# Kernel optimization log

Hardware: AMD Instinct MI355X
Metric: run time of the kernel (lower is better)

## Reference

```python
import jax, jax.numpy as jnp
import numpy as np

B, T, C = 4, 1024, 1024
H, D = 16, 64


def setup_inputs() -> dict:
    key = jax.random.key(0)
    ks = jax.random.split(key, 5)
    sc = 0.02
    x = jax.random.normal(ks[0], (B, T, C), dtype=jnp.float32)
    Wq = jax.random.normal(ks[1], (H, C, D), dtype=jnp.float32) * sc
    Wk = jax.random.normal(ks[2], (H, C, D), dtype=jnp.float32) * sc
    Wv = jax.random.normal(ks[3], (H, C, D), dtype=jnp.float32) * sc
    Wp = jax.random.normal(ks[4], (H * D, C), dtype=jnp.float32) * sc
    bp = jnp.zeros((C,), dtype=jnp.float32)
    return {"x": x, "Wq": Wq, "Wk": Wk, "Wv": Wv, "Wp": Wp, "bp": bp}


def reference(x, Wq, Wk, Wv, Wp, bp):
    # per-head projections (bias-free, as in nanoGPT Head)
    q = jnp.einsum('btc,hcd->bhtd', x, Wq)
    k = jnp.einsum('btc,hcd->bhtd', x, Wk)
    v = jnp.einsum('btc,hcd->bhtd', x, Wv)
    scale = 1.0 / jnp.sqrt(jnp.asarray(D, dtype=x.dtype))
    scores = jnp.einsum('bhtd,bhsd->bhts', q, k) * scale  # [B,H,T,T]
    causal = jnp.tril(jnp.ones((T, T), dtype=bool))
    scores = jnp.where(causal, scores, jnp.asarray(-jnp.inf, dtype=scores.dtype))
    attn = jax.nn.softmax(scores, axis=-1)
    out = jnp.einsum('bhts,bhsd->bhtd', attn, v)  # [B,H,T,D]
    out = out.transpose(0, 2, 1, 3).reshape(B, T, H * D)  # concat heads
    return out @ Wp + bp  # final projection (dropout=0)
```

## Files before the change

### kernel.cpp

```cpp
#include <hip/hip_runtime.h>
#include <hip/hip_bf16.h>

typedef unsigned short u16;
typedef __bf16 bf16x8 __attribute__((ext_vector_type(8)));
typedef float floatx4 __attribute__((ext_vector_type(4)));

#define SB 4
#define ST 1024
#define SC 1024
#define SH 16
#define SD 64

__device__ __forceinline__ u16 f2bf(float f) {
    unsigned int u = __builtin_bit_cast(unsigned int, f);
    u += 0x7fffu + ((u >> 16) & 1u);
    return (u16)(u >> 16);
}

__device__ __forceinline__ void gload16(const u16* g, u16* l) {
    __builtin_amdgcn_global_load_lds(
        (const __attribute__((address_space(1))) unsigned int*)g,
        (__attribute__((address_space(3))) unsigned int*)l, 16, 0, 0);
}

__global__ void k_cvt_x(const float* __restrict__ x, u16* __restrict__ xb, int n4) {
    int i = blockIdx.x * blockDim.x + threadIdx.x;
    if (i < n4) {
        float4 v = ((const float4*)x)[i];
        uint2 o;
        o.x = (unsigned)f2bf(v.x) | ((unsigned)f2bf(v.y) << 16);
        o.y = (unsigned)f2bf(v.z) | ((unsigned)f2bf(v.w) << 16);
        ((uint2*)xb)[i] = o;
    }
}

__global__ void k_cvt_wqkv(const float* __restrict__ Wq, const float* __restrict__ Wk,
                           const float* __restrict__ Wv, u16* __restrict__ Wt) {
    __shared__ float tile[64][65];
    const int qkv = blockIdx.z, h = blockIdx.y, c0 = blockIdx.x * 64;
    const float* src = qkv == 0 ? Wq : (qkv == 1 ? Wk : Wv);
    #pragma unroll
    for (int i = 0; i < 16; ++i) {
        int idx = threadIdx.x + i * 256;
        int r = idx >> 6, d = idx & 63;
        tile[r][d] = src[(h * SC + c0 + r) * SD + d];
    }
    __syncthreads();
    #pragma unroll
    for (int i = 0; i < 16; ++i) {
        int idx = threadIdx.x + i * 256;
        int d = idx >> 6, cc = idx & 63;
        Wt[(qkv * 1024 + h * SD + d) * SC + c0 + cc] = f2bf(tile[cc][d]);
    }
}

__global__ void k_cvt_wp(const float* __restrict__ Wp, u16* __restrict__ Wt) {
    __shared__ float tile[64][65];
    const int n0 = blockIdx.x * 64, k0 = blockIdx.y * 64;
    #pragma unroll
    for (int i = 0; i < 16; ++i) {
        int idx = threadIdx.x + i * 256;
        int r = idx >> 6, nn = idx & 63;
        tile[r][nn] = Wp[(k0 + r) * SC + n0 + nn];
    }
    __syncthreads();
    #pragma unroll
    for (int i = 0; i < 16; ++i) {
        int idx = threadIdx.x + i * 256;
        int nr = idx >> 6, kk = idx & 63;
        Wt[(n0 + nr) * (SH * SD) + k0 + kk] = f2bf(tile[kk][nr]);
    }
}

__global__ void k_tv(const u16* __restrict__ V, u16* __restrict__ Vt) {
    __shared__ u16 tl[64 * 72];
    const int bh = blockIdx.y, t0 = blockIdx.x * 64;
    const int tid = threadIdx.x;
    #pragma unroll
    for (int i = 0; i < 2; ++i) {
        int idx = tid + i * 256;
        int r = idx >> 3, c = idx & 7;
        *(uint4*)&tl[r * 72 + c * 8] = *(const uint4*)&V[((long)bh * ST + t0 + r) * SD + c * 8];
    }
    __syncthreads();
    #pragma unroll
    for (int i = 0; i < 2; ++i) {
        int idx = tid + i * 256;
        int d = idx >> 3, tc = idx & 7;
        u16 tmp[8];
        #pragma unroll
        for (int e = 0; e < 8; ++e) tmp[e] = tl[(tc * 8 + e) * 72 + d];
        *(uint4*)&Vt[((long)bh * SD + d) * ST + t0 + tc * 8] = *(uint4*)tmp;
    }
}

template<int BN, int MODE>
__launch_bounds__(256)
__global__ void k_gemm(const u16* __restrict__ A, const u16* __restrict__ Bt,
                       int M, int N, int K,
                       u16* __restrict__ Qb, u16* __restrict__ Kb, u16* __restrict__ Vb,
                       const float* __restrict__ bias, float* __restrict__ Cout) {
    constexpr int SN = BN / 32, CB = BN / 32;
    __shared__ u16 Als[128 * 64];
    __shared__ u16 Bls[BN * 64];
    const int tid = threadIdx.x, lane = tid & 63, w = tid >> 6;
    const int quad = lane >> 4, l16 = lane & 15;
    const int sr = lane >> 3, sc = lane & 7;
    const int nt = N / BN;
    const int m0 = (blockIdx.x / nt) * 128, n0 = (blockIdx.x % nt) * BN;
    const int wm = (w >> 1) * 64, wn = (w & 1) * (BN / 2);

    floatx4 acc[4][SN] = {};
    for (int k0 = 0; k0 < K; k0 += 64) {
        #pragma unroll
        for (int i = 0; i < 4; ++i) {
            int rb = (w * 4 + i) * 8;
            gload16(&A[(long)(m0 + rb + sr) * K + k0 + ((sc ^ sr) << 3)], &Als[rb * 64]);
        }
        #pragma unroll
        for (int i = 0; i < CB; ++i) {
            int rb = (w * CB + i) * 8;
            gload16(&Bt[(long)(n0 + rb + sr) * K + k0 + ((sc ^ sr) << 3)], &Bls[rb * 64]);
        }
        __syncthreads();
        bf16x8 af[4][2], bfr[SN][2];
        #pragma unroll
        for (int sm = 0; sm < 4; ++sm) {
            int row = wm + sm * 16 + l16;
            #pragma unroll
            for (int ks = 0; ks < 2; ++ks)
                af[sm][ks] = *(const bf16x8*)&Als[row * 64 + (((ks * 4 + quad) ^ (row & 7)) << 3)];
        }
        #pragma unroll
        for (int sn = 0; sn < SN; ++sn) {
            int row = wn + sn * 16 + l16;
            #pragma unroll
            for (int ks = 0; ks < 2; ++ks)
                bfr[sn][ks] = *(const bf16x8*)&Bls[row * 64 + (((ks * 4 + quad) ^ (row & 7)) << 3)];
        }
        #pragma unroll
        for (int ks = 0; ks < 2; ++ks)
            #pragma unroll
            for (int sm = 0; sm < 4; ++sm)
                #pragma unroll
                for (int sn = 0; sn < SN; ++sn)
                    acc[sm][sn] = __builtin_amdgcn_mfma_f32_16x16x32_bf16(af[sm][ks], bfr[sn][ks], acc[sm][sn], 0, 0, 0);
        __syncthreads();
    }
    #pragma unroll
    for (int sm = 0; sm < 4; ++sm) {
        #pragma unroll
        for (int sn = 0; sn < SN; ++sn) {
            #pragma unroll
            for (int r = 0; r < 4; ++r) {
                int m = m0 + wm + sm * 16 + quad * 4 + r;
                int n = n0 + wn + sn * 16 + l16;
                float v = acc[sm][sn][r];
                if (MODE == 0) {
                    int qkv = n >> 10, rem = n & 1023, h = rem >> 6, d = rem & 63;
                    int b = m >> 10, t = m & 1023;
                    if (qkv == 0) v *= 0.18033688011112042f;
                    u16* dst = qkv == 0 ? Qb : (qkv == 1 ? Kb : Vb);
                    dst[(((b * SH + h) * ST + t) << 6) + d] = f2bf(v);
                } else {
                    Cout[(long)m * N + n] = v + bias[n];
                }
            }
        }
    }
}

__launch_bounds__(256)
__global__ void k_attn(const u16* __restrict__ Qg, const u16* __restrict__ Kg,
                       const u16* __restrict__ Vtg, u16* __restrict__ Og) {
    __shared__ u16 Kls[64 * 64];
    __shared__ u16 Vls[64 * 64];
    __shared__ u16 Pls[64 * 64];
    const int tid = threadIdx.x, lane = tid & 63, w = tid >> 6;
    const int quad = lane >> 4, l16 = lane & 15;
    const int sr = lane >> 3, sc = lane & 7;
    const int id = blockIdx.x;
    const int bh = id & 63, pr = id >> 6;
    const int b = bh >> 4, h = bh & 15;
    const u16* Qbh = Qg + (long)bh * ST * SD;
    const u16* Kbh = Kg + (long)bh * ST * SD;
    const u16* Vbh = Vtg + (long)bh * SD * ST;

    #pragma unroll
    for (int ti = 0; ti < 2; ++ti) {
        const int tile = ti == 0 ? (15 - pr) : pr;
        const int t0 = tile * 64;
        bf16x8 qf[2];
        {
            const u16* qrow = Qbh + (t0 + w * 16 + l16) * SD;
            qf[0] = *(const bf16x8*)&qrow[quad * 8];
            qf[1] = *(const bf16x8*)&qrow[32 + quad * 8];
        }
        floatx4 oacc[4] = {};
        float lsum[4] = {};

        for (int j = 0; j <= tile; ++j) {
            const int s0 = j * 64;
            #pragma unroll
            for (int i = 0; i < 2; ++i) {
                int rb = (w * 2 + i) * 8;
                gload16(&Kbh[(s0 + rb + sr) * SD + ((sc ^ sr) << 3)], &Kls[rb * 64]);
                gload16(&Vbh[(rb + sr) * ST + s0 + ((sc ^ sr) << 3)], &Vls[rb * 64]);
            }
            __syncthreads();

            floatx4 sa[4] = {};
            #pragma unroll
            for (int sn = 0; sn < 4; ++sn) {
                int row = sn * 16 + l16;
                #pragma unroll
                for (int ks = 0; ks < 2; ++ks) {
                    bf16x8 kf = *(const bf16x8*)&Kls[row * 64 + (((ks * 4 + quad) ^ (row & 7)) << 3)];
                    sa[sn] = __builtin_amdgcn_mfma_f32_16x16x32_bf16(qf[ks], kf, sa[sn], 0, 0, 0);
                }
            }
            const bool diag = (j == tile);
            #pragma unroll
            for (int sn = 0; sn < 4; ++sn) {
                const int scol = s0 + sn * 16 + l16;
                const int c = sn * 2 + (l16 >> 3);
                #pragma unroll
                for (int r = 0; r < 4; ++r) {
                    const int rowP = w * 16 + quad * 4 + r;
                    float e = __builtin_exp2f(sa[sn][r]);
                    if (diag && scol > t0 + rowP - w * 16 + w * 16) e = 0.f;
                    lsum[r] += e;
                    Pls[rowP * 64 + ((c ^ (rowP & 7)) << 3) + (l16 & 7)] =
                        (u16)(__builtin_bit_cast(unsigned int, e) >> 16);
                }
            }
            bf16x8 pf[2];
            {
                int row = w * 16 + l16;
                #pragma unroll
                for (int ks = 0; ks < 2; ++ks)
                    pf[ks] = *(const bf16x8*)&Pls[row * 64 + (((ks * 4 + quad) ^ (row & 7)) << 3)];
            }
            #pragma unroll
            for (int dn = 0; dn < 4; ++dn) {
                int row = dn * 16 + l16;
                #pragma unroll
                for (int ks = 0; ks < 2; ++ks) {
                    bf16x8 vf = *(const bf16x8*)&Vls[row * 64 + (((ks * 4 + quad) ^ (row & 7)) << 3)];
                    oacc[dn] = __builtin_amdgcn_mfma_f32_16x16x32_bf16(pf[ks], vf, oacc[dn], 0, 0, 0);
                }
            }
            __syncthreads();
        }
        #pragma unroll
        for (int r = 0; r < 4; ++r) {
            float l = lsum[r];
            l += __shfl_xor(l, 1);
            l += __shfl_xor(l, 2);
            l += __shfl_xor(l, 4);
            l += __shfl_xor(l, 8);
            const float inv = 1.0f / l;
            const int t = t0 + w * 16 + quad * 4 + r;
            #pragma unroll
            for (int dn = 0; dn < 4; ++dn)
                Og[((long)(b * ST + t) << 10) + h * SD + dn * 16 + l16] = f2bf(oacc[dn][r] * inv);
        }
    }
}

extern "C" void kernel_launch(void* const* d_in, const int* in_sizes, int n_in,
                              void* d_out, int out_size, void* d_ws, size_t ws_size,
                              hipStream_t stream) {
    const float* x  = (const float*)d_in[0];
    const float* Wq = (const float*)d_in[1];
    const float* Wk = (const float*)d_in[2];
    const float* Wv = (const float*)d_in[3];
    const float* Wp = (const float*)d_in[4];
    const float* bp = (const float*)d_in[5];
    float* out = (float*)d_out;

    char* ws = (char*)d_ws;
    u16* xb   = (u16*)(ws);
    u16* Wqkv = (u16*)(ws + (8ll  << 20));
    u16* Wpt  = (u16*)(ws + (14ll << 20));
    u16* Qb   = (u16*)(ws + (16ll << 20));
    u16* Kb   = (u16*)(ws + (24ll << 20));
    u16* Vb   = (u16*)(ws + (32ll << 20));
    u16* Ob   = (u16*)(ws + (40ll << 20));
    u16* Vt   = (u16*)(ws);

    k_cvt_x<<<4096, 256, 0, stream>>>(x, xb, SB * ST * SC / 4);
    k_cvt_wqkv<<<dim3(16, 16, 3), 256, 0, stream>>>(Wq, Wk, Wv, Wqkv);
    k_cvt_wp<<<dim3(16, 16), 256, 0, stream>>>(Wp, Wpt);
    k_gemm<128, 0><<<32 * 24, 256, 0, stream>>>(xb, Wqkv, 4096, 3072, 1024, Qb, Kb, Vb, nullptr, nullptr);
    k_tv<<<dim3(16, 64), 256, 0, stream>>>(Vb, Vt);
    k_attn<<<512, 256, 0, stream>>>(Qb, Kb, Vt, Ob);
    k_gemm<64, 1><<<32 * 16, 256, 0, stream>>>(Ob, Wpt, 4096, 1024, 1024, nullptr, nullptr, nullptr, bp, out);
}
```

Before: 182.8 us.

## Swap MFMA operands for vectorized epilogues, shrink GEMM tiles, split attention tiles

The MFMA operand order is swapped in the GEMMs and in attention, so each lane holds 4 consecutive columns. That allows packed uint2 bf16 stores and float4 output/bias stores in place of scalar stores, and lets the P tile be written to LDS in packed form. The GEMM tiles shrink (QKV 128x64, projection 64x64), which doubles the block count. The attention kernel now runs one query tile per block over 1024 blocks instead of a balanced pair per block over 512. The aim is higher occupancy and fewer store instructions, at the cost of more redundant operand loads per block and uneven causal work per block.

```diff
diff --git a/kernel.cpp b/kernel.cpp
--- a/kernel.cpp
+++ b/kernel.cpp
@@ -94,38 +94,38 @@
     }
 }
 
-template<int BN, int MODE>
+template<int BM, int BN, int MODE>
 __launch_bounds__(256)
 __global__ void k_gemm(const u16* __restrict__ A, const u16* __restrict__ Bt,
                        int M, int N, int K,
                        u16* __restrict__ Qb, u16* __restrict__ Kb, u16* __restrict__ Vb,
                        const float* __restrict__ bias, float* __restrict__ Cout) {
-    constexpr int SN = BN / 32, CB = BN / 32;
-    __shared__ u16 Als[128 * 64];
+    constexpr int SM = BM / 32, SN = BN / 32;
+    __shared__ u16 Als[BM * 64];
     __shared__ u16 Bls[BN * 64];
     const int tid = threadIdx.x, lane = tid & 63, w = tid >> 6;
     const int quad = lane >> 4, l16 = lane & 15;
     const int sr = lane >> 3, sc = lane & 7;
     const int nt = N / BN;
-    const int m0 = (blockIdx.x / nt) * 128, n0 = (blockIdx.x % nt) * BN;
-    const int wm = (w >> 1) * 64, wn = (w & 1) * (BN / 2);
-
-    floatx4 acc[4][SN] = {};
+    const int m0 = (blockIdx.x / nt) * BM, n0 = (blockIdx.x % nt) * BN;
+    const int wm = (w >> 1) * (BM / 2), wn = (w & 1) * (BN / 2);
+
+    floatx4 acc[SM][SN] = {};
     for (int k0 = 0; k0 < K; k0 += 64) {
         #pragma unroll
-        for (int i = 0; i < 4; ++i) {
-            int rb = (w * 4 + i) * 8;
+        for (int i = 0; i < BM / 32; ++i) {
+            int rb = (w * (BM / 32) + i) * 8;
             gload16(&A[(long)(m0 + rb + sr) * K + k0 + ((sc ^ sr) << 3)], &Als[rb * 64]);
         }
         #pragma unroll
-        for (int i = 0; i < CB; ++i) {
-            int rb = (w * CB + i) * 8;
+        for (int i = 0; i < BN / 32; ++i) {
+            int rb = (w * (BN / 32) + i) * 8;
             gload16(&Bt[(long)(n0 + rb + sr) * K + k0 + ((sc ^ sr) << 3)], &Bls[rb * 64]);
         }
         __syncthreads();
-        bf16x8 af[4][2], bfr[SN][2];
-        #pragma unroll
-        for (int sm = 0; sm < 4; ++sm) {
+        bf16x8 af[SM][2], bfr[SN][2];
+        #pragma unroll
+        for (int sm = 0; sm < SM; ++sm) {
             int row = wm + sm * 16 + l16;
             #pragma unroll
             for (int ks = 0; ks < 2; ++ks)
@@ -141,30 +141,43 @@
         #pragma unroll
         for (int ks = 0; ks < 2; ++ks)
             #pragma unroll
-            for (int sm = 0; sm < 4; ++sm)
+            for (int sm = 0; sm < SM; ++sm)
                 #pragma unroll
                 for (int sn = 0; sn < SN; ++sn)
-                    acc[sm][sn] = __builtin_amdgcn_mfma_f32_16x16x32_bf16(af[sm][ks], bfr[sn][ks], acc[sm][sn], 0, 0, 0);
+                    acc[sm][sn] = __builtin_amdgcn_mfma_f32_16x16x32_bf16(bfr[sn][ks], af[sm][ks], acc[sm][sn], 0, 0, 0);
         __syncthreads();
     }
-    #pragma unroll
-    for (int sm = 0; sm < 4; ++sm) {
+    if (MODE == 0) {
+        const int qkv = n0 >> 10, h = (n0 & 1023) >> 6;
+        u16* dst = qkv == 0 ? Qb : (qkv == 1 ? Kb : Vb);
+        const float qs = qkv == 0 ? 0.18033688011112042f : 1.0f;
+        #pragma unroll
+        for (int sm = 0; sm < SM; ++sm) {
+            const int m = m0 + wm + sm * 16 + l16;
+            const long base = ((long)((m >> 10) * SH + h) * ST + (m & 1023)) << 6;
+            #pragma unroll
+            for (int sn = 0; sn < SN; ++sn) {
+                const int d0 = (wn + sn * 16 + (quad << 2)) & 63;
+                u16 pk[4];
+                #pragma unroll
+                for (int r = 0; r < 4; ++r) pk[r] = f2bf(acc[sm][sn][r] * qs);
+                *(uint2*)&dst[base + d0] = *(uint2*)pk;
+            }
+        }
+    } else {
         #pragma unroll
         for (int sn = 0; sn < SN; ++sn) {
-            #pragma unroll
-            for (int r = 0; r < 4; ++r) {
-                int m = m0 + wm + sm * 16 + quad * 4 + r;
-                int n = n0 + wn + sn * 16 + l16;
-                float v = acc[sm][sn][r];
-                if (MODE == 0) {
-                    int qkv = n >> 10, rem = n & 1023, h = rem >> 6, d = rem & 63;
-                    int b = m >> 10, t = m & 1023;
-                    if (qkv == 0) v *= 0.18033688011112042f;
-                    u16* dst = qkv == 0 ? Qb : (qkv == 1 ? Kb : Vb);
-                    dst[(((b * SH + h) * ST + t) << 6) + d] = f2bf(v);
-                } else {
-                    Cout[(long)m * N + n] = v + bias[n];
-                }
+            const int nb = n0 + wn + sn * 16 + (quad << 2);
+            const float4 bv = *(const float4*)&bias[nb];
+            #pragma unroll
+            for (int sm = 0; sm < SM; ++sm) {
+                const int m = m0 + wm + sm * 16 + l16;
+                float4 o;
+                o.x = acc[sm][sn][0] + bv.x;
+                o.y = acc[sm][sn][1] + bv.y;
+                o.z = acc[sm][sn][2] + bv.z;
+                o.w = acc[sm][sn][3] + bv.w;
+                *(float4*)&Cout[(long)m * N + nb] = o;
             }
         }
     }
@@ -179,92 +192,85 @@
     const int tid = threadIdx.x, lane = tid & 63, w = tid >> 6;
     const int quad = lane >> 4, l16 = lane & 15;
     const int sr = lane >> 3, sc = lane & 7;
-    const int id = blockIdx.x;
-    const int bh = id & 63, pr = id >> 6;
+    const int tile = 15 - (blockIdx.x >> 6);
+    const int bh = blockIdx.x & 63;
+    const int t0 = tile * 64;
     const int b = bh >> 4, h = bh & 15;
     const u16* Qbh = Qg + (long)bh * ST * SD;
     const u16* Kbh = Kg + (long)bh * ST * SD;
     const u16* Vbh = Vtg + (long)bh * SD * ST;
 
-    #pragma unroll
-    for (int ti = 0; ti < 2; ++ti) {
-        const int tile = ti == 0 ? (15 - pr) : pr;
-        const int t0 = tile * 64;
-        bf16x8 qf[2];
-        {
-            const u16* qrow = Qbh + (t0 + w * 16 + l16) * SD;
-            qf[0] = *(const bf16x8*)&qrow[quad * 8];
-            qf[1] = *(const bf16x8*)&qrow[32 + quad * 8];
-        }
-        floatx4 oacc[4] = {};
-        float lsum[4] = {};
-
-        for (int j = 0; j <= tile; ++j) {
-            const int s0 = j * 64;
-            #pragma unroll
-            for (int i = 0; i < 2; ++i) {
-                int rb = (w * 2 + i) * 8;
-                gload16(&Kbh[(s0 + rb + sr) * SD + ((sc ^ sr) << 3)], &Kls[rb * 64]);
-                gload16(&Vbh[(rb + sr) * ST + s0 + ((sc ^ sr) << 3)], &Vls[rb * 64]);
-            }
-            __syncthreads();
-
-            floatx4 sa[4] = {};
-            #pragma unroll
-            for (int sn = 0; sn < 4; ++sn) {
-                int row = sn * 16 + l16;
-                #pragma unroll
-                for (int ks = 0; ks < 2; ++ks) {
-                    bf16x8 kf = *(const bf16x8*)&Kls[row * 64 + (((ks * 4 + quad) ^ (row & 7)) << 3)];
-                    sa[sn] = __builtin_amdgcn_mfma_f32_16x16x32_bf16(qf[ks], kf, sa[sn], 0, 0, 0);
-                }
-            }
-            const bool diag = (j == tile);
-            #pragma unroll
-            for (int sn = 0; sn < 4; ++sn) {
-                const int scol = s0 + sn * 16 + l16;
-                const int c = sn * 2 + (l16 >> 3);
-                #pragma unroll
-                for (int r = 0; r < 4; ++r) {
-                    const int rowP = w * 16 + quad * 4 + r;
-                    float e = __builtin_exp2f(sa[sn][r]);
-                    if (diag && scol > t0 + rowP - w * 16 + w * 16) e = 0.f;
-                    lsum[r] += e;
-                    Pls[rowP * 64 + ((c ^ (rowP & 7)) << 3) + (l16 & 7)] =
-                        (u16)(__builtin_bit_cast(unsigned int, e) >> 16);
-                }
-            }
-            bf16x8 pf[2];
-            {
-                int row = w * 16 + l16;
-                #pragma unroll
-                for (int ks = 0; ks < 2; ++ks)
-                    pf[ks] = *(const bf16x8*)&Pls[row * 64 + (((ks * 4 + quad) ^ (row & 7)) << 3)];
-            }
-            #pragma unroll
-            for (int dn = 0; dn < 4; ++dn) {
-                int row = dn * 16 + l16;
-                #pragma unroll
-                for (int ks = 0; ks < 2; ++ks) {
-                    bf16x8 vf = *(const bf16x8*)&Vls[row * 64 + (((ks * 4 + quad) ^ (row & 7)) << 3)];
-                    oacc[dn] = __builtin_amdgcn_mfma_f32_16x16x32_bf16(pf[ks], vf, oacc[dn], 0, 0, 0);
-                }
-            }
-            __syncthreads();
-        }
-        #pragma unroll
-        for (int r = 0; r < 4; ++r) {
-            float l = lsum[r];
-            l += __shfl_xor(l, 1);
-            l += __shfl_xor(l, 2);
-            l += __shfl_xor(l, 4);
-            l += __shfl_xor(l, 8);
-            const float inv = 1.0f / l;
-            const int t = t0 + w * 16 + quad * 4 + r;
-            #pragma unroll
-            for (int dn = 0; dn < 4; ++dn)
-                Og[((long)(b * ST + t) << 10) + h * SD + dn * 16 + l16] = f2bf(oacc[dn][r] * inv);
-        }
+    bf16x8 qf[2];
+    {
+        const u16* qrow = Qbh + (t0 + w * 16 + l16) * SD;
+        qf[0] = *(const bf16x8*)&qrow[quad * 8];
+        qf[1] = *(const bf16x8*)&qrow[32 + quad * 8];
+    }
+    floatx4 oacc[4] = {};
+    float lsum = 0.f;
+    const int myt = t0 + w * 16 + l16;
+    const int rowP = w * 16 + l16;
+
+    for (int j = 0; j <= tile; ++j) {
+        const int s0 = j * 64;
+        #pragma unroll
+        for (int i = 0; i < 2; ++i) {
+            int rb = (w * 2 + i) * 8;
+            gload16(&Kbh[(s0 + rb + sr) * SD + ((sc ^ sr) << 3)], &Kls[rb * 64]);
+            gload16(&Vbh[(rb + sr) * ST + s0 + ((sc ^ sr) << 3)], &Vls[rb * 64]);
+        }
+        __syncthreads();
+
+        floatx4 sa[4] = {};
+        #pragma unroll
+        for (int sn = 0; sn < 4; ++sn) {
+            int row = sn * 16 + l16;
+            #pragma unroll
+            for (int ks = 0; ks < 2; ++ks) {
+                bf16x8 kf = *(const bf16x8*)&Kls[row * 64 + (((ks * 4 + quad) ^ (row & 7)) << 3)];
+                sa[sn] = __builtin_amdgcn_mfma_f32_16x16x32_bf16(kf, qf[ks], sa[sn], 0, 0, 0);
+            }
+        }
+        const bool diag = (j == tile);
+        #pragma unroll
+        for (int sn = 0; sn < 4; ++sn) {
+            const int sl = sn * 16 + (quad << 2);
+            u16 pk[4];
+            #pragma unroll
+            for (int r = 0; r < 4; ++r) {
+                float e = __builtin_exp2f(sa[sn][r]);
+                if (diag && s0 + sl + r > myt) e = 0.f;
+                lsum += e;
+                pk[r] = (u16)(__builtin_bit_cast(unsigned int, e) >> 16);
+            }
+            *(uint2*)&Pls[rowP * 64 + ((((sl >> 3)) ^ (rowP & 7)) << 3) + ((quad & 1) << 2)] = *(uint2*)pk;
+        }
+        bf16x8 pf[2];
+        #pragma unroll
+        for (int ks = 0; ks < 2; ++ks)
+            pf[ks] = *(const bf16x8*)&Pls[rowP * 64 + (((ks * 4 + quad) ^ (rowP & 7)) << 3)];
+        #pragma unroll
+        for (int dn = 0; dn < 4; ++dn) {
+            int row = dn * 16 + l16;
+            #pragma unroll
+            for (int ks = 0; ks < 2; ++ks) {
+                bf16x8 vf = *(const bf16x8*)&Vls[row * 64 + (((ks * 4 + quad) ^ (row & 7)) << 3)];
+                oacc[dn] = __builtin_amdgcn_mfma_f32_16x16x32_bf16(vf, pf[ks], oacc[dn], 0, 0, 0);
+            }
+        }
+        __syncthreads();
+    }
+    float l = lsum;
+    l += __shfl_xor(l, 16);
+    l += __shfl_xor(l, 32);
+    const float inv = 1.0f / l;
+    const long obase = ((long)(b * ST + myt) << 10) + h * SD;
+    #pragma unroll
+    for (int dn = 0; dn < 4; ++dn) {
+        u16 pk[4];
+        #pragma unroll
+        for (int r = 0; r < 4; ++r) pk[r] = f2bf(oacc[dn][r] * inv);
+        *(uint2*)&Og[obase + dn * 16 + (quad << 2)] = *(uint2*)pk;
     }
 }
 
@@ -292,8 +298,8 @@
     k_cvt_x<<<4096, 256, 0, stream>>>(x, xb, SB * ST * SC / 4);
     k_cvt_wqkv<<<dim3(16, 16, 3), 256, 0, stream>>>(Wq, Wk, Wv, Wqkv);
     k_cvt_wp<<<dim3(16, 16), 256, 0, stream>>>(Wp, Wpt);
-    k_gemm<128, 0><<<32 * 24, 256, 0, stream>>>(xb, Wqkv, 4096, 3072, 1024, Qb, Kb, Vb, nullptr, nullptr);
+    k_gemm<128, 64, 0><<<32 * 48, 256, 0, stream>>>(xb, Wqkv, 4096, 3072, 1024, Qb, Kb, Vb, nullptr, nullptr);
     k_tv<<<dim3(16, 64), 256, 0, stream>>>(Vb, Vt);
-    k_attn<<<512, 256, 0, stream>>>(Qb, Kb, Vt, Ob);
-    k_gemm<64, 1><<<32 * 16, 256, 0, stream>>>(Ob, Wpt, 4096, 1024, 1024, nullptr, nullptr, nullptr, bp, out);
-}
+    k_attn<<<1024, 256, 0, stream>>>(Qb, Kb, Vt, Ob);
+    k_gemm<64, 64, 1><<<64 * 16, 256, 0, stream>>>(Ob, Wpt, 4096, 1024, 1024, nullptr, nullptr, nullptr, bp, out);
+}
```

Result: no change. 179.6 us (-1.7%).
